# Performance work log

Hardware: AMD Instinct MI355X
Metric: run time of the kernel (lower is better)

Reference implementation:

```python
import jax, jax.numpy as jnp
import numpy as np

STAGE_SHAPES = {
    'stage1': [(12, 10, 3, 3), (12, 12, 3, 3), (12, 12, 3, 3)],
    'stage2': [(24, 22, 3, 3), (24, 24, 3, 3), (12, 24, 3, 3)],
    'stage3': [(24, 22, 3, 3), (24, 24, 3, 3), (12, 24, 3, 3)],
    'stage4': [(11, 22, 1, 1)],
}
BN_CH = [12, 12, 12, 24, 24, 12, 24, 24, 12]  # channels of the 9 BN layers, in forward order
OFF = np.concatenate([[0], np.cumsum(BN_CH)]).tolist()
EPS = 1e-5


def _split_weights(wflat, shapes):
    """Slice flat [B, P] hypernet weights into per-layer [B, O, I, k, k] tensors."""
    outs, bg = [], 0
    for s in shapes:
        n = int(np.prod(s))
        outs.append(wflat[:, bg:bg + n].reshape((-1,) + s))
        bg += n
    return outs


def _per_sample_conv(x, w):
    """x: [B, C, H, W], w: [B, O, C, k, k] -> [B, O, H, W]. Each sample uses its own filters (SAME padding = k//2 for odd k)."""
    def one(xi, wi):
        return jax.lax.conv_general_dilated(
            xi[None], wi, window_strides=(1, 1), padding='SAME',
            dimension_numbers=('NCHW', 'OIHW', 'NCHW'))[0]
    return jax.vmap(one)(x, w)


def _bn_eval(y, gamma, beta, mean, var):
    """Eval-mode BatchNorm2d over channel dim of [B, C, H, W]."""
    inv = gamma * jax.lax.rsqrt(var + EPS)
    return y * inv[None, :, None, None] + (beta - mean * inv)[None, :, None, None]


def setup_inputs():
    key = jax.random.key(0)
    ks = jax.random.split(key, 8)
    B, H, W = 64, 128, 128
    x = jax.random.normal(ks[0], (B, 10, H, W), jnp.float32)
    # scale hypernet weights down so 9 stacked convs stay numerically tame
    w_stage1 = jax.random.normal(ks[1], (B, 3672), jnp.float32) * 0.05
    w_stage2 = jax.random.normal(ks[2], (B, 12528), jnp.float32) * 0.05
    w_stage3 = jax.random.normal(ks[3], (B, 12528), jnp.float32) * 0.05
    w_stage4 = jax.random.normal(ks[4], (B, 242), jnp.float32) * 0.05
    n_bn = sum(BN_CH)  # 144
    bn_gamma = jax.random.uniform(ks[5], (n_bn,), jnp.float32, 0.5, 1.5)
    bn_beta = jax.random.normal(ks[6], (n_bn,), jnp.float32) * 0.1
    bn_mean = jnp.zeros((n_bn,), jnp.float32)
    bn_var = jnp.ones((n_bn,), jnp.float32)
    return dict(x=x, w_stage1=w_stage1, w_stage2=w_stage2, w_stage3=w_stage3,
                w_stage4=w_stage4, bn_gamma=bn_gamma, bn_beta=bn_beta,
                bn_mean=bn_mean, bn_var=bn_var)


def reference(x, w_stage1, w_stage2, w_stage3, w_stage4, bn_gamma, bn_beta, bn_mean, bn_var):
    cur = x
    li = 0  # global BN layer index
    for stage_key, wflat in (('stage1', w_stage1), ('stage2', w_stage2), ('stage3', w_stage3)):
        for w in _split_weights(wflat, STAGE_SHAPES[stage_key]):
            conv = _per_sample_conv(cur, w)
            lo, hi = OFF[li], OFF[li + 1]
            bn = _bn_eval(conv, bn_gamma[lo:hi], bn_beta[lo:hi], bn_mean[lo:hi], bn_var[lo:hi])
            cur = jax.nn.relu(bn)
            li += 1
        cur = jnp.concatenate([cur, x], axis=1)  # dense skip: [B, 12+10, H, W]
    w_pred = _split_weights(w_stage4, STAGE_SHAPES['stage4'])[0]  # [B, 11, 22, 1, 1]
    return _per_sample_conv(cur, w_pred)
```

## Files before the change

### kernel.cpp

```cpp
#include <hip/hip_runtime.h>
#include <stdint.h>

#define HW    16384
#define NB    64
#define W2    130
#define PXS   (W2*W2)
#define WQH   70144
#define EPSB  1e-5f
#define GP    1444
#define GPB   23104
#define ROWB  608
#define PLH   34656
#define NTH   768
#define NWV   12

typedef _Float16 h8  __attribute__((ext_vector_type(8)));
typedef _Float16 h4  __attribute__((ext_vector_type(4)));
typedef float    f16v __attribute__((ext_vector_type(16)));
typedef float    f4  __attribute__((ext_vector_type(4)));
typedef h8 uh8 __attribute__((aligned(4)));
typedef h4 uh4 __attribute__((aligned(4)));
typedef f4 uf4 __attribute__((aligned(4)));

__global__ void prep_w(const float* __restrict__ w1, const float* __restrict__ w2,
                       const float* __restrict__ w3, const float* __restrict__ w4,
                       const float* __restrict__ g,  const float* __restrict__ be,
                       const float* __restrict__ mu, const float* __restrict__ va,
                       _Float16* __restrict__ wq, float* __restrict__ bias)
{
    const int FO[11]   = {0,576,1152,1728,2880,4032,5184,6336,7488,8640,8768};
    const int start[10]= {0,1080,2376,3672,8424,13608,16200,20952,26136,28728};
    const int COt[10]  = {12,12,12,24,24,12,24,24,12,11};
    const int CIt[10]  = {10,12,12,22,24,24,22,24,24,22};
    const int bnoff[10]= {0,12,24,36,60,84,96,120,144,0};
    const int KST[10]  = {1,1,1,2,2,2,2,2,2,2};

    long tid = (long)blockIdx.x * 256 + threadIdx.x;
    long total = (long)NB * 8768, stride = (long)gridDim.x * 256;
    for (long idx = tid; idx < total; idx += stride) {
        int b = (int)(idx / 8768), i = (int)(idx - (long)b * 8768);
        int l = 9; while (i < FO[l]) --l;
        int j = i - FO[l];
        int f = j >> 6, lane = j & 63;
        int ks = (KST[l] == 2) ? (f & 1) : 0;
        int s  = (KST[l] == 2) ? (f >> 1) : f;
        int co = lane & 31, hi = lane >> 5;
        int CO = COt[l], CI = CIt[l];
        float scale = 1.f;
        if (l < 9 && co < CO) {
            int bi = bnoff[l] + co;
            scale = g[bi] * rsqrtf(va[bi] + EPSB);
        }
        int c0 = ks * 16 + hi * 8;
        __attribute__((aligned(16))) _Float16 vals[8];
#pragma unroll
        for (int e = 0; e < 8; ++e) {
            int c = c0 + e; float wv = 0.f;
            if (co < CO && c < CI) {
                int p = (l < 9) ? start[l] + (co * CI + c) * 9 + s
                                : start[9] + co * CI + c;
                const float* src; long si;
                if      (p <  3672) { src = w1; si = (long)b *  3672 + p; }
                else if (p < 16200) { src = w2; si = (long)b * 12528 + (p -  3672); }
                else if (p < 28728) { src = w3; si = (long)b * 12528 + (p - 16200); }
                else                { src = w4; si = (long)b *   242 + (p - 28728); }
                wv = src[si] * scale;
            }
            vals[e] = (_Float16)wv;
        }
        *(uh8*)(wq + idx * 8) = *(const h8*)vals;
    }
    if (tid < 320) {
        int l = (int)tid >> 5, co = (int)tid & 31;
        float v = 0.f;
        if (l < 9 && co < COt[l]) {
            int bi = bnoff[l] + co;
            float sc = g[bi] * rsqrtf(va[bi] + EPSB);
            v = be[bi] - mu[bi] * sc;
        }
        bias[tid] = v;
    }
}

__global__ void pad_x(const float* __restrict__ x, _Float16* __restrict__ bufA,
                      _Float16* __restrict__ bufB, int b0)
{
    int sl = blockIdx.x >> 3, part = blockIdx.x & 7;
    int gb = b0 + sl;
    const float* __restrict__ xs = x + (long)gb * 10 * HW;
    _Float16* __restrict__ dA = bufA + (long)sl * PXS * 32;
    _Float16* __restrict__ dB = bufB + (long)sl * PXS * 32;
    for (int p = part * 256 + threadIdx.x; p < PXS; p += 2048) {
        int r = p / W2, cc = p - r * W2;
        __attribute__((aligned(16))) _Float16 pxA[32], pxB[32];
#pragma unroll
        for (int i = 0; i < 32; ++i) { pxA[i] = (_Float16)0.f; pxB[i] = (_Float16)0.f; }
        if (r >= 1 && r <= 128 && cc >= 1 && cc <= 128) {
            int so = (r - 1) * 128 + (cc - 1);
#pragma unroll
            for (int c = 0; c < 10; ++c) {
                _Float16 xv = (_Float16)xs[c * HW + so];
                pxA[c] = xv; pxA[12 + c] = xv; pxB[12 + c] = xv;
            }
        }
        _Float16* ap = dA + (long)p * 32;
        _Float16* bp = dB + (long)p * 32;
#pragma unroll
        for (int q = 0; q < 4; ++q) {
            *(uh8*)(ap + q * 8) = *(const h8*)(pxA + q * 8);
            *(uh8*)(bp + q * 8) = *(const h8*)(pxB + q * 8);
        }
    }
}

template<int KST, int NR>
__device__ __forceinline__ void lconv(const char* pin, char* pout,
    const _Float16* wl, const float* __restrict__ bias, int boff,
    int rowStart, int nRows, int colStart, int width,
    int oy0, int ox0, int w, int lo5, int hi)
{
    constexpr int qmax = (KST == 1) ? 2 : 3;
    constexpr int NG = 3 * KST;
    constexpr int FR = 9 * KST;

    h8 afr[FR];
#pragma unroll
    for (int f = 0; f < FR; ++f) afr[f] = *(const uh8*)(wl + (long)f * 512);

    const int ncb = (width > 32) ? 2 : 1;
    const int nrg = (nRows + NR - 1) / NR;
    const int nu  = nrg * ncb;
#pragma unroll 1
    for (int u = w; u < nu; u += NWV) {
        int rg, cb;
        if (ncb == 2) { rg = u >> 1; cb = u & 1; } else { rg = u; cb = 0; }
        int r0 = rowStart + rg * NR;
        { int rmax = rowStart + nRows - NR; r0 = (r0 > rmax) ? rmax : r0; }
        const int cs   = cb ? (colStart + width - 32) : colStart;
        const int cmin = cb ? (64 - width) : 0;
        const char* bin = pin + (long)hi * GPB
                        + ((long)(r0 - 1) * 38 + (cs - 1 + lo5)) * 16;

        f16v acc[NR];
        { f16v z = {};
#pragma unroll
          for (int i = 0; i < NR; ++i) acc[i] = z; }

#pragma unroll
        for (int g = 0; g < NG; ++g) {
            const int kc = g / KST, ks = g - kc * KST;
            h8 bf[NR + 2];
#pragma unroll
            for (int j = 0; j < NR + 2; ++j) {
                h8 v = {};
                if (!(ks & hi))
                    v = *(const uh8*)(bin + ks * 2 * GPB + kc * 16 + j * ROWB);
                bf[j] = v;
            }
#pragma unroll
            for (int kr = 0; kr < 3; ++kr)
#pragma unroll
                for (int tt = 0; tt < NR; ++tt)
                    acc[tt] = __builtin_amdgcn_mfma_f32_32x32x16_f16(
                                  afr[(kr * 3 + kc) * KST + ks], bf[kr + tt], acc[tt], 0, 0, 0);
        }

        f4 bv[qmax];
#pragma unroll
        for (int q = 0; q < qmax; ++q) bv[q] = *(const uf4*)(bias + boff + hi * 4 + q * 8);
        const bool cok = (lo5 >= cmin);
        const int  pc  = cs + lo5;
        const int  gx  = ox0 - 3 + pc;
        const bool xin = (unsigned)(gx - 1) < 128u;
        char* pob = pout + (long)hi * 8 + ((long)r0 * 38 + pc) * 16;
        if (cok) {
#pragma unroll
            for (int tt = 0; tt < NR; ++tt) {
                int gy = oy0 - 3 + r0 + tt;
                bool ok = xin && ((unsigned)(gy - 1) < 128u);
#pragma unroll
                for (int q = 0; q < qmax; ++q) {
                    float v0 = ok ? fmaxf(acc[tt][4*q+0] + bv[q][0], 0.f) : 0.f;
                    float v1 = ok ? fmaxf(acc[tt][4*q+1] + bv[q][1], 0.f) : 0.f;
                    float v2 = ok ? fmaxf(acc[tt][4*q+2] + bv[q][2], 0.f) : 0.f;
                    float v3 = ok ? fmaxf(acc[tt][4*q+3] + bv[q][3], 0.f) : 0.f;
                    h4 hv = { (_Float16)v0, (_Float16)v1, (_Float16)v2, (_Float16)v3 };
                    *(uh4*)(pob + q * GPB + tt * ROWB) = hv;
                }
            }
        }
    }
}

template<int KST>
__global__ __launch_bounds__(NTH)
void stage3(const _Float16* __restrict__ in, _Float16* __restrict__ out,
            const _Float16* __restrict__ wq, int loff0,
            const float* __restrict__ bias, int boff0, int b0)
{
    __shared__ _Float16 lds[2][PLH];
    const int t = threadIdx.x, w = t >> 6, l = t & 63;
    const int lo5 = l & 31, hi = l >> 5;

    const int nbb = (int)(gridDim.x >> 4);
    int s, tile;
    if ((nbb & 7) == 0) {
        int xcd = (int)(blockIdx.x & 7), j = (int)(blockIdx.x >> 3);
        s = xcd * (nbb >> 3) + (j >> 4); tile = j & 15;
    } else { s = (int)(blockIdx.x >> 4); tile = (int)(blockIdx.x & 15); }
    const int gb  = b0 + s;
    const int oy0 = 1 + (tile >> 2) * 32;
    const int ox0 = 1 + (tile & 3) * 32;

    {
        const char* src = (const char*)(in + (long)s * PXS * 32);
        char* dst = (char*)&lds[0][0];
        h8 stg[6];
#pragma unroll
        for (int k = 0; k < 6; ++k) {
            int idx = k * NTH + t;
            int p = idx / 3, c = idx - p * 3;
            int r = p / 38, cc = p - r * 38;
            int gy = oy0 - 3 + r, gx = ox0 - 3 + cc;
            h8 v = {};
            if (idx < 3 * GP && (unsigned)gy < 130u && (unsigned)gx < 130u)
                v = *(const uh8*)(src + ((long)gy * W2 + gx) * 64 + c * 16);
            stg[k] = v;
        }
#pragma unroll
        for (int k = 0; k < 6; ++k) {
            int idx = k * NTH + t;
            int p = idx / 3, c = idx - p * 3;
            if (idx < 3 * GP)
                *(uh8*)(dst + (long)c * GPB + (long)p * 16) = stg[k];
        }
    }
    __syncthreads();

    const _Float16* wl = wq + (long)gb * WQH + loff0 + (long)l * 8;
    constexpr int LSTEP = 9 * KST * 512;
    lconv<KST,3>((const char*)lds[0], (char*)lds[1], wl,             bias, boff0,      1, 36, 1, 36, oy0, ox0, w, lo5, hi);
    __syncthreads();
    lconv<KST,3>((const char*)lds[1], (char*)lds[0], wl + LSTEP,     bias, boff0 + 32, 2, 34, 2, 34, oy0, ox0, w, lo5, hi);
    __syncthreads();
    lconv<KST,3>((const char*)lds[0], (char*)lds[1], wl + 2 * LSTEP, bias, boff0 + 64, 3, 32, 3, 32, oy0, ox0, w, lo5, hi);
    __syncthreads();

    {
        _Float16* db = out + (long)s * PXS * 32;
        const char* T = (const char*)&lds[1][0];
#pragma unroll
        for (int k = 0; k < 2; ++k) {
            int px = k * NTH + t;
            if (px < 1024) {
                int pr = 3 + (px >> 5), pc = 3 + (px & 31);
                int gy = oy0 + (px >> 5), gx = ox0 + (px & 31);
                const char* sp = T + ((long)pr * 38 + pc) * 16;
                h8 v0 = *(const uh8*)sp;
                h4 v1 = *(const uh4*)(sp + GPB);
                _Float16* dp = db + ((long)gy * W2 + gx) * 32;
                *(uh8*)dp = v0;
                *(uh4*)(dp + 8) = v1;
            }
        }
    }
}

__global__ __launch_bounds__(256, 2)
void conv1(const _Float16* __restrict__ in, float* __restrict__ outF,
           const _Float16* __restrict__ wq, int loff, int b0)
{
    const int s = blockIdx.y, gb = b0 + s;
    const int t = threadIdx.x, w = t >> 6, l = t & 63;
    const int lo5 = l & 31, hi = l >> 5;
    const int cb = blockIdx.x & 3;
    const int y00 = (blockIdx.x >> 2) * 32 + w * 8;
    const int xpix = cb * 32 + lo5;

    const _Float16* wl = wq + (long)gb * WQH + loff + (long)l * 8;
    h8 a0 = *(const uh8*)(wl);
    h8 a1 = *(const uh8*)(wl + 512);
    const _Float16* ib = in + (long)s * PXS * 32;

#pragma unroll 1
    for (int tt = 0; tt < 8; ++tt) {
        int y = y00 + tt;
        const _Float16* bp = ib + ((long)(y + 1) * W2 + xpix + 1) * 32 + hi * 8;
        h8 bA = *(const uh8*)(bp);
        h8 bB = *(const uh8*)(bp + 16);
        f16v acc = {};
        acc = __builtin_amdgcn_mfma_f32_32x32x16_f16(a0, bA, acc, 0, 0, 0);
        acc = __builtin_amdgcn_mfma_f32_32x32x16_f16(a1, bB, acc, 0, 0, 0);
        long px = (long)y * 128 + xpix;
#pragma unroll
        for (int r = 0; r < 16; ++r) {
            int co = (r & 3) + 8 * (r >> 2) + 4 * hi;
            if (co < 11) outF[((long)gb * 11 + co) * HW + px] = acc[r];
        }
    }
}

extern "C" void kernel_launch(void* const* d_in, const int* in_sizes, int n_in,
                              void* d_out, int out_size, void* d_ws, size_t ws_size,
                              hipStream_t stream)
{
    const float *x = (const float*)d_in[0], *w1 = (const float*)d_in[1],
                *w2 = (const float*)d_in[2], *w3 = (const float*)d_in[3],
                *w4 = (const float*)d_in[4], *g  = (const float*)d_in[5],
                *be = (const float*)d_in[6], *mu = (const float*)d_in[7],
                *va = (const float*)d_in[8];
    if (n_in == 9) {
        const float* big801[2] = {nullptr, nullptr}; int n801 = 0;
        const float* bn156[4]  = {nullptr, nullptr, nullptr, nullptr}; int n156 = 0;
        const float *fx = nullptr, *fw1 = nullptr, *fw4 = nullptr;
        for (int i = 0; i < 9; ++i) {
            int sz = in_sizes[i];
            if      (sz == 10485760) fx  = (const float*)d_in[i];
            else if (sz ==   235008) fw1 = (const float*)d_in[i];
            else if (sz ==   801792) { if (n801 < 2) big801[n801++] = (const float*)d_in[i]; }
            else if (sz ==    15488) fw4 = (const float*)d_in[i];
            else if (sz ==      156) { if (n156 < 4) bn156[n156++] = (const float*)d_in[i]; }
        }
        if (fx && fw1 && fw4 && n801 == 2 && n156 == 4) {
            x = fx; w1 = fw1; w2 = big801[0]; w3 = big801[1]; w4 = fw4;
            g = bn156[0]; be = bn156[1]; mu = bn156[2]; va = bn156[3];
        }
    }
    float* out = (float*)d_out;

    const size_t wqB   = (size_t)NB * WQH * 2;
    const size_t biasB = 2048;
    const size_t hdr   = wqB + biasB;
    const size_t perSlot = (size_t)PXS * 128;
    size_t avail = ws_size > hdr ? ws_size - hdr : 0;
    int chunk = (int)(avail / perSlot);
    if (chunk > NB) chunk = NB;
    if (chunk < 1)  chunk = 1;

    _Float16* wq   = (_Float16*)d_ws;
    float*    bias = (float*)((char*)d_ws + wqB);
    _Float16* bufA = (_Float16*)((char*)d_ws + hdr);
    _Float16* bufB = bufA + (size_t)chunk * PXS * 32;

    prep_w<<<2048, 256, 0, stream>>>(w1, w2, w3, w4, g, be, mu, va, wq, bias);

    for (int b0 = 0; b0 < NB; b0 += chunk) {
        int nb = (NB - b0 < chunk) ? (NB - b0) : chunk;
        pad_x<<<nb * 8, 256, 0, stream>>>(x, bufA, bufB, b0);
        int gc = nb * 16;
        dim3 g1(16, nb);
        stage3<1><<<gc, NTH, 0, stream>>>(bufA, bufB, wq,     0, bias,   0, b0);
        stage3<2><<<gc, NTH, 0, stream>>>(bufB, bufA, wq, 13824, bias,  96, b0);
        stage3<2><<<gc, NTH, 0, stream>>>(bufA, bufB, wq, 41472, bias, 192, b0);
        conv1<<<g1, 256, 0, stream>>>(bufB, out, wq, 69120, b0);
    }
}
```

Before: 466.5 us.

## Size LDS per stage, zero-page branchless loads, interleave wave phases with setprio

Stage kernels now size LDS by the number of channel groups actually used, so KST=1 uses two groups and launches with 1024 threads. The per-element branch that zeroed the second k-step for upper-half lanes is replaced by pointing those lanes at a small zeroed LDS page, which makes the B-fragment loads unconditional. Odd waves walk the k-groups in reverse order, and the MFMA bursts are wrapped in s_setprio, so different waves hit LDS and the matrix unit at different times. The costs are an extra zero page in LDS, code duplication from the two template variants, and register pressure from the 1024-thread launch.

```diff
diff --git a/kernel.cpp b/kernel.cpp
--- a/kernel.cpp
+++ b/kernel.cpp
@@ -10,9 +10,7 @@
 #define GP    1444
 #define GPB   23104
 #define ROWB  608
-#define PLH   34656
-#define NTH   768
-#define NWV   12
+#define ZPB   2560
 
 typedef _Float16 h8  __attribute__((ext_vector_type(8)));
 typedef _Float16 h4  __attribute__((ext_vector_type(4)));
@@ -113,8 +111,9 @@
     }
 }
 
-template<int KST, int NR>
+template<int KST, int NR, int TNWV, bool REV>
 __device__ __forceinline__ void lconv(const char* pin, char* pout,
+    const char* zbase,
     const _Float16* wl, const float* __restrict__ bias, int boff,
     int rowStart, int nRows, int colStart, int width,
     int oy0, int ox0, int w, int lo5, int hi)
@@ -131,7 +130,7 @@
     const int nrg = (nRows + NR - 1) / NR;
     const int nu  = nrg * ncb;
 #pragma unroll 1
-    for (int u = w; u < nu; u += NWV) {
+    for (int u = w; u < nu; u += TNWV) {
         int rg, cb;
         if (ncb == 2) { rg = u >> 1; cb = u & 1; } else { rg = u; cb = 0; }
         int r0 = rowStart + rg * NR;
@@ -140,6 +139,8 @@
         const int cmin = cb ? (64 - width) : 0;
         const char* bin = pin + (long)hi * GPB
                         + ((long)(r0 - 1) * 38 + (cs - 1 + lo5)) * 16;
+        const char* binH = bin + 2 * GPB;
+        if (KST == 2 && hi) binH = zbase;
 
         f16v acc[NR];
         { f16v z = {};
@@ -147,22 +148,22 @@
           for (int i = 0; i < NR; ++i) acc[i] = z; }
 
 #pragma unroll
-        for (int g = 0; g < NG; ++g) {
+        for (int gg = 0; gg < NG; ++gg) {
+            const int g  = REV ? (NG - 1 - gg) : gg;
             const int kc = g / KST, ks = g - kc * KST;
+            const char* base = ks ? binH : bin;
             h8 bf[NR + 2];
 #pragma unroll
-            for (int j = 0; j < NR + 2; ++j) {
-                h8 v = {};
-                if (!(ks & hi))
-                    v = *(const uh8*)(bin + ks * 2 * GPB + kc * 16 + j * ROWB);
-                bf[j] = v;
-            }
+            for (int j = 0; j < NR + 2; ++j)
+                bf[j] = *(const uh8*)(base + kc * 16 + j * ROWB);
+            __builtin_amdgcn_s_setprio(1);
 #pragma unroll
             for (int kr = 0; kr < 3; ++kr)
 #pragma unroll
                 for (int tt = 0; tt < NR; ++tt)
                     acc[tt] = __builtin_amdgcn_mfma_f32_32x32x16_f16(
                                   afr[(kr * 3 + kc) * KST + ks], bf[kr + tt], acc[tt], 0, 0, 0);
+            __builtin_amdgcn_s_setprio(0);
         }
 
         f4 bv[qmax];
@@ -192,13 +193,18 @@
     }
 }
 
-template<int KST>
-__global__ __launch_bounds__(NTH)
+template<int KST, int TNTH>
+__global__ __launch_bounds__(TNTH)
 void stage3(const _Float16* __restrict__ in, _Float16* __restrict__ out,
             const _Float16* __restrict__ wq, int loff0,
             const float* __restrict__ bias, int boff0, int b0)
 {
-    __shared__ _Float16 lds[2][PLH];
+    constexpr int NGR  = (KST == 1) ? 2 : 3;
+    constexpr int PLHk = NGR * GP * 8;
+    constexpr int TNWV = TNTH / 64;
+    __shared__ _Float16 lds[2][PLHk];
+    __shared__ char zpad[(KST == 2) ? ZPB : 16];
+
     const int t = threadIdx.x, w = t >> 6, l = t & 63;
     const int lo5 = l & 31, hi = l >> 5;
 
@@ -213,45 +219,60 @@
     const int ox0 = 1 + (tile & 3) * 32;
 
     {
+        constexpr int NLD = NGR * GP;
+        constexpr int SI  = (NLD + TNTH - 1) / TNTH;
         const char* src = (const char*)(in + (long)s * PXS * 32);
         char* dst = (char*)&lds[0][0];
-        h8 stg[6];
-#pragma unroll
-        for (int k = 0; k < 6; ++k) {
-            int idx = k * NTH + t;
-            int p = idx / 3, c = idx - p * 3;
+        h8 stg[SI];
+#pragma unroll
+        for (int k = 0; k < SI; ++k) {
+            int idx = k * TNTH + t;
+            int p = idx / NGR, c = idx - p * NGR;
             int r = p / 38, cc = p - r * 38;
             int gy = oy0 - 3 + r, gx = ox0 - 3 + cc;
             h8 v = {};
-            if (idx < 3 * GP && (unsigned)gy < 130u && (unsigned)gx < 130u)
+            if (idx < NLD && (unsigned)gy < 130u && (unsigned)gx < 130u)
                 v = *(const uh8*)(src + ((long)gy * W2 + gx) * 64 + c * 16);
             stg[k] = v;
         }
 #pragma unroll
-        for (int k = 0; k < 6; ++k) {
-            int idx = k * NTH + t;
-            int p = idx / 3, c = idx - p * 3;
-            if (idx < 3 * GP)
+        for (int k = 0; k < SI; ++k) {
+            int idx = k * TNTH + t;
+            int p = idx / NGR, c = idx - p * NGR;
+            if (idx < NLD)
                 *(uh8*)(dst + (long)c * GPB + (long)p * 16) = stg[k];
         }
+        if (KST == 2 && t < ZPB / 16) {
+            h8 z = {};
+            *(uh8*)(zpad + t * 16) = z;
+        }
     }
     __syncthreads();
 
     const _Float16* wl = wq + (long)gb * WQH + loff0 + (long)l * 8;
+    const char* zb = (const char*)zpad;
     constexpr int LSTEP = 9 * KST * 512;
-    lconv<KST,3>((const char*)lds[0], (char*)lds[1], wl,             bias, boff0,      1, 36, 1, 36, oy0, ox0, w, lo5, hi);
+#define LCONV(PIN, POUT, WOFF, BOFF, RS, NRW, CS, WD)                          \
+    if (w & 1) lconv<KST,3,TNWV,true >((const char*)(PIN), (char*)(POUT), zb,  \
+        wl + (WOFF), bias, boff0 + (BOFF), RS, NRW, CS, WD, oy0, ox0, w, lo5, hi); \
+    else       lconv<KST,3,TNWV,false>((const char*)(PIN), (char*)(POUT), zb,  \
+        wl + (WOFF), bias, boff0 + (BOFF), RS, NRW, CS, WD, oy0, ox0, w, lo5, hi);
+
+    LCONV(lds[0], lds[1], 0,         0,  1, 36, 1, 36);
     __syncthreads();
-    lconv<KST,3>((const char*)lds[1], (char*)lds[0], wl + LSTEP,     bias, boff0 + 32, 2, 34, 2, 34, oy0, ox0, w, lo5, hi);
+    LCONV(lds[1], lds[0], LSTEP,     32, 2, 34, 2, 34);
     __syncthreads();
-    lconv<KST,3>((const char*)lds[0], (char*)lds[1], wl + 2 * LSTEP, bias, boff0 + 64, 3, 32, 3, 32, oy0, ox0, w, lo5, hi);
+    LCONV(lds[0], lds[1], 2 * LSTEP, 64, 3, 32, 3, 32);
     __syncthreads();
+#undef LCONV
 
     {
         _Float16* db = out + (long)s * PXS * 32;
         const char* T = (const char*)&lds[1][0];
-#pragma unroll
-        for (int k = 0; k < 2; ++k) {
-            int px = k * NTH + t;
+        constexpr int WB = (1024 + TNTH - 1) / TNTH;
+#pragma unroll
+        for (int k = 0; k < WB; ++k) {
+            int px = k * TNTH + t;
             if (px < 1024) {
                 int pr = 3 + (px >> 5), pc = 3 + (px & 31);
                 int gy = oy0 + (px >> 5), gx = ox0 + (px & 31);
@@ -349,9 +370,9 @@
         pad_x<<<nb * 8, 256, 0, stream>>>(x, bufA, bufB, b0);
         int gc = nb * 16;
         dim3 g1(16, nb);
-        stage3<1><<<gc, NTH, 0, stream>>>(bufA, bufB, wq,     0, bias,   0, b0);
-        stage3<2><<<gc, NTH, 0, stream>>>(bufB, bufA, wq, 13824, bias,  96, b0);
-        stage3<2><<<gc, NTH, 0, stream>>>(bufA, bufB, wq, 41472, bias, 192, b0);
+        stage3<1,1024><<<gc, 1024, 0, stream>>>(bufA, bufB, wq,     0, bias,   0, b0);
+        stage3<2, 768><<<gc,  768, 0, stream>>>(bufB, bufA, wq, 13824, bias,  96, b0);
+        stage3<2, 768><<<gc,  768, 0, stream>>>(bufA, bufB, wq, 41472, bias, 192, b0);
         conv1<<<g1, 256, 0, stream>>>(bufB, out, wq, 69120, b0);
     }
 }
```

Result: no change. 461.1 us (-1.2%).
